# Optimization experiments

Hardware: AMD Instinct MI355X
Metric: run time of the kernel (lower is better)

The kernel has to match this reference:

```python
import jax, jax.numpy as jnp
import numpy as np

EMBED_DIM = 1024
NUM_HEAD = 16
HEAD_DIM = EMBED_DIM // NUM_HEAD
B, T = 4, 2048


def setup_inputs() -> dict:
    key = jax.random.key(0)
    ks = jax.random.split(key, 6)
    s_in = 1.0 / np.sqrt(EMBED_DIM)
    return {
        "hidden_states": jax.random.normal(ks[0], (B, T, EMBED_DIM), dtype=jnp.float32),
        "attn_mask": jnp.ones((B, T), dtype=jnp.int32),
        "W_qkv": jax.random.uniform(ks[1], (3 * EMBED_DIM, EMBED_DIM), jnp.float32, -s_in, s_in),
        "b_qkv": jax.random.uniform(ks[2], (3 * EMBED_DIM,), jnp.float32, -s_in, s_in),
        "W_o": jax.random.uniform(ks[3], (EMBED_DIM, EMBED_DIM), jnp.float32, -s_in, s_in),
        "b_o": jax.random.uniform(ks[4], (EMBED_DIM,), jnp.float32, -s_in, s_in),
    }


def reference(hidden_states, attn_mask, W_qkv, b_qkv, W_o, b_o):
    Bb, Tt, C = hidden_states.shape
    H, D = NUM_HEAD, HEAD_DIM
    scaling = D ** (-0.5)

    qkv = hidden_states @ W_qkv.T + b_qkv  # [B,T,3C]
    q, k, v = jnp.split(qkv, 3, axis=-1)
    # [B,H,T,D]
    q = q.reshape(Bb, Tt, H, D).transpose(0, 2, 1, 3)
    k = k.reshape(Bb, Tt, H, D).transpose(0, 2, 1, 3)
    v = v.reshape(Bb, Tt, H, D).transpose(0, 2, 1, 3)

    scores = jnp.einsum("bhqd,bhkd->bhqk", q, k) * scaling  # [B,H,T,T]

    causal = jnp.tril(jnp.ones((Tt, Tt), dtype=bool))[None, None]  # [1,1,T,T]
    am = attn_mask.astype(bool)
    mask = causal & am[:, None, :, None] & am[:, None, None, :]  # [B,1,T,T]
    scores = jnp.where(mask, scores, -jnp.inf)

    probs = jax.nn.softmax(scores, axis=-1)
    out = jnp.einsum("bhqk,bhkd->bhqd", probs, v)  # [B,H,T,D]
    out = out.transpose(0, 2, 1, 3).reshape(Bb, Tt, C)
    return out @ W_o.T + b_o
```

## Files before the change

kernel.cpp:

```cpp
#include <hip/hip_runtime.h>
#include <cstdint>
#include <cstddef>
#include <math.h>

#define BATCH 4
#define TSEQ  2048
#define CDIM  1024
#define NH    16
#define HDIM  64
#define MTOT  (BATCH * TSEQ)


typedef __attribute__((ext_vector_type(4))) float  floatx4;
typedef __attribute__((ext_vector_type(8))) short  shortx8;
typedef __attribute__((ext_vector_type(4))) short  shortx4;

__device__ __forceinline__ short f2bf(float f) {
    union { float f; unsigned int u; } v; v.f = f;
    unsigned int lsb = (v.u >> 16) & 1u;
    v.u += 0x7fffu + lsb;
    return (short)(v.u >> 16);
}

#if defined(__has_builtin)
#  if __has_builtin(__builtin_amdgcn_exp2f)
#    define EXP2F(x) __builtin_amdgcn_exp2f(x)
#  else
#    define EXP2F(x) exp2f(x)
#  endif
#  if __has_builtin(__builtin_amdgcn_perm)
__device__ __forceinline__ unsigned pack_hi16(unsigned hi, unsigned lo) {
    return __builtin_amdgcn_perm(hi, lo, 0x07060302u);
}
#  else
__device__ __forceinline__ unsigned pack_hi16(unsigned hi, unsigned lo) {
    return (lo >> 16) | (hi & 0xffff0000u);
}
#  endif
#  if __has_builtin(__builtin_amdgcn_mfma_f32_16x16x16bf16_1k)
#    define HAS_MFMA_1K 1
#  else
#    define HAS_MFMA_1K 0
#  endif
#else
#  define EXP2F(x) exp2f(x)
__device__ __forceinline__ unsigned pack_hi16(unsigned hi, unsigned lo) {
    return (lo >> 16) | (hi & 0xffff0000u);
}
#  define HAS_MFMA_1K 0
#endif

#define QSCALE (0.125f * 1.44269504088896f)

__global__ __launch_bounds__(256) void cvt_kernel(const float4* __restrict__ src,
                                                  shortx4* __restrict__ dst, int n4)
{
    int i = blockIdx.x * 256 + threadIdx.x;
    if (i < n4) {
        float4 v = src[i];
        shortx4 s;
        s[0] = f2bf(v.x); s[1] = f2bf(v.y); s[2] = f2bf(v.z); s[3] = f2bf(v.w);
        dst[i] = s;
    }
}

__global__ __launch_bounds__(256) void cvt3_kernel(
    const float4* __restrict__ s1, shortx4* __restrict__ d1,
    const float4* __restrict__ s2, shortx4* __restrict__ d2,
    const float4* __restrict__ s3, shortx4* __restrict__ d3)
{
    int bid = blockIdx.x;
    const float4* s; shortx4* d; int i;
    if (bid < 8192)       { s = s1; d = d1; i = bid * 256 + threadIdx.x; }
    else if (bid < 11264) { s = s2; d = d2; i = (bid - 8192) * 256 + threadIdx.x; }
    else                  { s = s3; d = d3; i = (bid - 11264) * 256 + threadIdx.x; }
    float4 v = s[i];
    shortx4 o;
    o[0] = f2bf(v.x); o[1] = f2bf(v.y); o[2] = f2bf(v.z); o[3] = f2bf(v.w);
    d[i] = o;
}

__device__ __forceinline__ void stageA_bf16(const short* g, short* S, int row0,
                                            int K, int k0, int tid, int wave)
{
#pragma unroll
    for (int i = 0; i < 2; ++i) {
        int c = i * 256 + tid;
        int r = c >> 2, kc = c & 3;
        __builtin_amdgcn_global_load_lds(
            (__attribute__((address_space(1))) void*)(g + (size_t)(row0 + r) * K + k0 + kc * 8),
            (__attribute__((address_space(3))) void*)((char*)S + i * 4096 + wave * 1024),
            16, 0, 0);
    }
}
__device__ __forceinline__ void stageB_f32(const float* g, short* S, int row0,
                                           int K, int k0, int tid)
{
#pragma unroll
    for (int i = 0; i < 4; ++i) {
        int c = i * 256 + tid;
        int r = c >> 3, fc = c & 7;
        const float4 v = *(const float4*)(g + (size_t)(row0 + r) * K + k0 + fc * 4);
        shortx4 s4;
        s4[0] = f2bf(v.x); s4[1] = f2bf(v.y); s4[2] = f2bf(v.z); s4[3] = f2bf(v.w);
        *(shortx4*)(S + r * 32 + fc * 4) = s4;
    }
}

__device__ __forceinline__ void qkv_epilogue(
    floatx4 (&acc)[4][4], const float* bias,
    short* Qo, short* Ko, short* VTo,
    int row0, int col0, int wr, int wc, int quad, int l16)
{
#pragma unroll
    for (int mi = 0; mi < 4; ++mi) {
        int m = row0 + wr * 64 + mi * 16 + quad * 4;
        int b = m >> 11, t0 = m & (TSEQ - 1);
#pragma unroll
        for (int ni = 0; ni < 4; ++ni) {
            int n = col0 + wc * 64 + ni * 16 + l16;
            float bv = bias[n];
            int part = n >> 10, rem = n & 1023;
            int h = rem >> 6, d = rem & 63;
            if (part == 2) {
                shortx4 st;
#pragma unroll
                for (int r = 0; r < 4; ++r) st[r] = f2bf(acc[mi][ni][r] + bv);
                *(shortx4*)(VTo + (((size_t)(b * NH + h)) * HDIM + d) * TSEQ + t0) = st;
            } else {
                short* dst = (part == 0) ? Qo : Ko;
                float scale = (part == 0) ? QSCALE : 1.0f;
#pragma unroll
                for (int r = 0; r < 4; ++r) {
                    size_t idx = (((size_t)(b * NH + h)) * TSEQ + (t0 + r)) * HDIM + d;
                    dst[idx] = f2bf((acc[mi][ni][r] + bv) * scale);
                }
            }
        }
    }
}

__global__ __launch_bounds__(256) void gemm_qkv_fast_kernel(
    const short* __restrict__ A,
    const short* __restrict__ W,
    const float* __restrict__ bias,
    short* __restrict__ Qo, short* __restrict__ Ko, short* __restrict__ VTo)
{
    __shared__ short As[128 * 32];
    __shared__ short Bs[128 * 32];
    const int tid  = threadIdx.x;
    const int lane = tid & 63, wave = tid >> 6;
    const int quad = lane >> 4, l16 = lane & 15;
    const int wr = wave >> 1, wc = wave & 1;
    const int row0 = blockIdx.x * 128;
    const int col0 = blockIdx.y * 128;
    const int K = CDIM;

    floatx4 acc[4][4] = {};

    for (int k0 = 0; k0 < K; k0 += 32) {
        stageA_bf16(A, As, row0, K, k0, tid, wave);
        stageA_bf16(W, Bs, col0, K, k0, tid, wave);
        __syncthreads();

        shortx8 af[4], bfr[4];
#pragma unroll
        for (int mi = 0; mi < 4; ++mi)
            af[mi] = *(const shortx8*)(As + (wr * 64 + mi * 16 + l16) * 32 + quad * 8);
#pragma unroll
        for (int ni = 0; ni < 4; ++ni)
            bfr[ni] = *(const shortx8*)(Bs + (wc * 64 + ni * 16 + l16) * 32 + quad * 8);
#pragma unroll
        for (int mi = 0; mi < 4; ++mi)
#pragma unroll
            for (int ni = 0; ni < 4; ++ni)
                acc[mi][ni] = __builtin_amdgcn_mfma_f32_16x16x32_bf16(
                    af[mi], bfr[ni], acc[mi][ni], 0, 0, 0);
        __syncthreads();
    }
    qkv_epilogue(acc, bias, Qo, Ko, VTo, row0, col0, wr, wc, quad, l16);
}

__global__ __launch_bounds__(256) void gemm_qkv_kernel(
    const short* __restrict__ A,
    const float* __restrict__ W,
    const float* __restrict__ bias,
    short* __restrict__ Qo, short* __restrict__ Ko, short* __restrict__ VTo)
{
    __shared__ short As[128 * 32];
    __shared__ short Bs[128 * 32];
    const int tid  = threadIdx.x;
    const int lane = tid & 63, wave = tid >> 6;
    const int quad = lane >> 4, l16 = lane & 15;
    const int wr = wave >> 1, wc = wave & 1;
    const int row0 = blockIdx.x * 128;
    const int col0 = blockIdx.y * 128;
    const int K = CDIM;

    floatx4 acc[4][4] = {};

    for (int k0 = 0; k0 < K; k0 += 32) {
        stageA_bf16(A, As, row0, K, k0, tid, wave);
        stageB_f32(W, Bs, col0, K, k0, tid);
        __syncthreads();

        shortx8 af[4], bfr[4];
#pragma unroll
        for (int mi = 0; mi < 4; ++mi)
            af[mi] = *(const shortx8*)(As + (wr * 64 + mi * 16 + l16) * 32 + quad * 8);
#pragma unroll
        for (int ni = 0; ni < 4; ++ni)
            bfr[ni] = *(const shortx8*)(Bs + (wc * 64 + ni * 16 + l16) * 32 + quad * 8);
#pragma unroll
        for (int mi = 0; mi < 4; ++mi)
#pragma unroll
            for (int ni = 0; ni < 4; ++ni)
                acc[mi][ni] = __builtin_amdgcn_mfma_f32_16x16x32_bf16(
                    af[mi], bfr[ni], acc[mi][ni], 0, 0, 0);
        __syncthreads();
    }
    qkv_epilogue(acc, bias, Qo, Ko, VTo, row0, col0, wr, wc, quad, l16);
}

__global__ __launch_bounds__(256) void attn_kernel(
    const short* __restrict__ Q,
    const short* __restrict__ Kg,
    const short* __restrict__ VT,
    const int*   __restrict__ am,
    short* __restrict__ O)
{
    __shared__ short Ks[128 * 64];
    __shared__ short Vs[64 * 128];

    const int tid  = threadIdx.x;
    const int lane = tid & 63, wave = tid >> 6;
    const int quad = lane >> 4, l16 = lane & 15;

    const int L = blockIdx.x;
    const int bh = (L & 7) + (((L >> 3) & 7) << 3);
    const int strip = 15 - (L >> 6);
    const int b = bh >> 4, h = bh & 15;

    const short* Qb = Q  + (size_t)bh * TSEQ * HDIM;
    const short* Kb = Kg + (size_t)bh * TSEQ * HDIM;
    const short* Vb = VT + (size_t)bh * HDIM * TSEQ;

    const int q0  = strip * 128;
    const int qb0 = q0 + wave * 32;
    const int qv0 = qb0 + l16;
    const int qv1 = qv0 + 16;

    shortx8 bq[2][2];
#pragma unroll
    for (int nq = 0; nq < 2; ++nq)
#pragma unroll
        for (int kk = 0; kk < 2; ++kk)
            bq[nq][kk] = *(const shortx8*)(
                Qb + (size_t)(qb0 + nq * 16 + l16) * HDIM + kk * 32 + quad * 8);

    floatx4 o[4][2] = {};
    floatx4 lacc[2] = {};

#if HAS_MFMA_1K
    const shortx4 ones4 = { (short)0x3F80, (short)0x3F80, (short)0x3F80, (short)0x3F80 };
#else
    const shortx8 ones8 = { (short)0x3F80, (short)0x3F80, (short)0x3F80, (short)0x3F80,
                            (short)0x3F80, (short)0x3F80, (short)0x3F80, (short)0x3F80 };
#endif

    const int ntiles = (q0 + 128) >> 7;
    for (int kt = 0; kt < ntiles; ++kt) {
        const int kt0 = kt << 7;
#pragma unroll
        for (int i = 0; i < 4; ++i) {
            int idx = i * 256 + tid;
            int rr = idx >> 3, cd = idx & 7;
            int cc = cd ^ (rr & 7);
            __builtin_amdgcn_global_load_lds(
                (__attribute__((address_space(1))) void*)(Kb + (size_t)(kt0 + rr) * HDIM + cc * 8),
                (__attribute__((address_space(3))) void*)((char*)Ks + i * 4096 + wave * 1024),
                16, 0, 0);
            int rrv = idx >> 4, cdv = idx & 15;
            int ccv = cdv ^ (rrv & 7);
            __builtin_amdgcn_global_load_lds(
                (__attribute__((address_space(1))) void*)(Vb + (size_t)rrv * TSEQ + kt0 + ccv * 8),
                (__attribute__((address_space(3))) void*)((char*)Vs + i * 4096 + wave * 1024),
                16, 0, 0);
        }
        int amv0 = am[b * TSEQ + kt0 + lane];
        int amv1 = am[b * TSEQ + kt0 + 64 + lane];
        __syncthreads();

#pragma unroll 1
        for (int p = 0; p < 2; ++p) {
            const int pb0 = kt0 + p * 64;
            int amv = p ? amv1 : amv0;
            bool allones = (__ballot(amv != 0) == 0xFFFFFFFFFFFFFFFFULL);

            floatx4 s[4][2] = {};
#pragma unroll
            for (int kk = 0; kk < 2; ++kk)
#pragma unroll
                for (int t = 0; t < 4; ++t) {
                    int rr = p * 64 + t * 16 + l16;
                    shortx8 kf = *(const shortx8*)(
                        Ks + rr * 64 + (((kk * 4 + quad) ^ (l16 & 7)) << 3));
#pragma unroll
                    for (int nq = 0; nq < 2; ++nq)
                        s[t][nq] = __builtin_amdgcn_mfma_f32_16x16x32_bf16(
                            kf, bq[nq][kk], s[t][nq], 0, 0, 0);
                }

            unsigned pk[4][2][2];
#pragma unroll
            for (int nq = 0; nq < 2; ++nq) {
                const int qv = nq ? qv1 : qv0;
#pragma unroll
                for (int t = 0; t < 4; ++t) {
                    bool diag = (pb0 + t * 16 + 15) > (qb0 + nq * 16);
                    unsigned pu[4];
#pragma unroll
                    for (int r = 0; r < 4; ++r) {
                        float pe = EXP2F(s[t][nq][r]);
                        unsigned u = __float_as_uint(pe) & 0xffff0000u;
                        if (!allones) {
                            int amr = __shfl(amv, t * 16 + quad * 4 + r);
                            u = amr ? u : 0u;
                        }
                        if (diag) {
                            int kv = pb0 + t * 16 + quad * 4 + r;
                            u = (kv <= qv) ? u : 0u;
                        }
                        pu[r] = u;
                    }
                    pk[t][nq][0] = pack_hi16(pu[1], pu[0]);
                    pk[t][nq][1] = pack_hi16(pu[3], pu[2]);
                }
            }

#if HAS_MFMA_1K
#pragma unroll
            for (int t = 0; t < 4; ++t) {
                union { unsigned u[2]; shortx4 s; } pb[2];
                pb[0].u[0] = pk[t][0][0]; pb[0].u[1] = pk[t][0][1];
                pb[1].u[0] = pk[t][1][0]; pb[1].u[1] = pk[t][1][1];
#pragma unroll
                for (int nq = 0; nq < 2; ++nq)
                    lacc[nq] = __builtin_amdgcn_mfma_f32_16x16x16bf16_1k(
                        ones4, pb[nq].s, lacc[nq], 0, 0, 0);
#pragma unroll
                for (int mi = 0; mi < 4; ++mi) {
                    int rr = mi * 16 + l16;
                    int cidx = (p * 8 + 2 * t + (quad >> 1)) ^ (l16 & 7);
                    shortx4 vf = *(const shortx4*)(Vs + rr * 128 + cidx * 8 + (quad & 1) * 4);
#pragma unroll
                    for (int nq = 0; nq < 2; ++nq)
                        o[mi][nq] = __builtin_amdgcn_mfma_f32_16x16x16bf16_1k(
                            vf, pb[nq].s, o[mi][nq], 0, 0, 0);
                }
            }
#else
#pragma unroll
            for (int kk2 = 0; kk2 < 2; ++kk2) {
                unsigned bfr[2][4];
#pragma unroll
                for (int nq = 0; nq < 2; ++nq)
#pragma unroll
                    for (int jj = 0; jj < 4; ++jj) {
                        int srclane = (((quad & 1) * 2 + (jj >> 1)) * 16 + l16) << 2;
                        int lo = __builtin_amdgcn_ds_bpermute(srclane, (int)pk[kk2 * 2][nq][jj & 1]);
                        int hi = __builtin_amdgcn_ds_bpermute(srclane, (int)pk[kk2 * 2 + 1][nq][jj & 1]);
                        bfr[nq][jj] = (quad >> 1) ? (unsigned)hi : (unsigned)lo;
                    }
                union { unsigned u[4]; shortx8 s; } pb[2];
#pragma unroll
                for (int nq = 0; nq < 2; ++nq) {
#pragma unroll
                    for (int jj = 0; jj < 4; ++jj) pb[nq].u[jj] = bfr[nq][jj];
                    lacc[nq] = __builtin_amdgcn_mfma_f32_16x16x32_bf16(
                        ones8, pb[nq].s, lacc[nq], 0, 0, 0);
                }
#pragma unroll
                for (int mi = 0; mi < 4; ++mi) {
                    int rr = mi * 16 + l16;
                    int cidx = (p * 8 + kk2 * 4 + quad) ^ (l16 & 7);
                    shortx8 vf8 = *(const shortx8*)(Vs + rr * 128 + cidx * 8);
#pragma unroll
                    for (int nq = 0; nq < 2; ++nq)
                        o[mi][nq] = __builtin_amdgcn_mfma_f32_16x16x32_bf16(
                            vf8, pb[nq].s, o[mi][nq], 0, 0, 0);
                }
            }
#endif
        }
        __syncthreads();
    }

#pragma unroll
    for (int nq = 0; nq < 2; ++nq) {
        float inv = 1.0f / lacc[nq][0];
        int q = qb0 + nq * 16 + l16;
#pragma unroll
        for (int mi = 0; mi < 4; ++mi) {
            shortx4 st;
#pragma unroll
            for (int r = 0; r < 4; ++r) st[r] = f2bf(o[mi][nq][r] * inv);
            *(shortx4*)(O + ((size_t)(b * TSEQ + q)) * CDIM + h * HDIM + mi * 16 + quad * 4) = st;
        }
    }
}

__global__ __launch_bounds__(256) void gemm_out_kernel(
    const short* __restrict__ A,
    const short* __restrict__ W,
    const float* __restrict__ bias,
    float* __restrict__ Out)
{
    __shared__ short As[128 * 32];
    __shared__ short Bs[128 * 32];
    const int tid  = threadIdx.x;
    const int lane = tid & 63, wave = tid >> 6;
    const int quad = lane >> 4, l16 = lane & 15;
    const int wr = wave >> 1, wc = wave & 1;
    const int row0 = blockIdx.x * 128;
    const int col0 = blockIdx.y * 128;
    const int K = CDIM;

    floatx4 acc[4][4] = {};

    for (int k0 = 0; k0 < K; k0 += 32) {
        stageA_bf16(A, As, row0, K, k0, tid, wave);
        stageA_bf16(W, Bs, col0, K, k0, tid, wave);
        __syncthreads();

        shortx8 af[4], bfr[4];
#pragma unroll
        for (int mi = 0; mi < 4; ++mi)
            af[mi] = *(const shortx8*)(As + (wr * 64 + mi * 16 + l16) * 32 + quad * 8);
#pragma unroll
        for (int ni = 0; ni < 4; ++ni)
            bfr[ni] = *(const shortx8*)(Bs + (wc * 64 + ni * 16 + l16) * 32 + quad * 8);
#pragma unroll
        for (int mi = 0; mi < 4; ++mi)
#pragma unroll
            for (int ni = 0; ni < 4; ++ni)
                acc[mi][ni] = __builtin_amdgcn_mfma_f32_16x16x32_bf16(
                    af[mi], bfr[ni], acc[mi][ni], 0, 0, 0);
        __syncthreads();
    }

#pragma unroll
    for (int mi = 0; mi < 4; ++mi) {
        int m = row0 + wr * 64 + mi * 16 + quad * 4;
#pragma unroll
        for (int ni = 0; ni < 4; ++ni) {
            int n = col0 + wc * 64 + ni * 16 + l16;
            float bv = bias[n];
#pragma unroll
            for (int r = 0; r < 4; ++r)
                Out[(size_t)(m + r) * CDIM + n] = acc[mi][ni][r] + bv;
        }
    }
}

extern "C" void kernel_launch(void* const* d_in, const int* in_sizes, int n_in,
                              void* d_out, int out_size, void* d_ws, size_t ws_size,
                              hipStream_t stream)
{
    const float* hs   = (const float*)d_in[0];
    const int*   am   = (const int*)d_in[1];
    const float* Wqkv = (const float*)d_in[2];
    const float* bqkv = (const float*)d_in[3];
    const float* Wo   = (const float*)d_in[4];
    const float* bo   = (const float*)d_in[5];
    float* out = (float*)d_out;

    char* ws = (char*)d_ws;
    short* slot = (short*)ws;
    short* Qw   = (short*)(ws + ((size_t)16 << 20));
    short* Kw   = (short*)(ws + ((size_t)32 << 20));
    short* VTw  = (short*)(ws + ((size_t)48 << 20));

    if (ws_size >= ((size_t)72 << 20)) {
        short* Wqkvb = (short*)(ws + ((size_t)64 << 20));
        short* Wob   = (short*)(ws + ((size_t)70 << 20));
        cvt3_kernel<<<dim3(12288), 256, 0, stream>>>(
            (const float4*)hs,   (shortx4*)slot,
            (const float4*)Wqkv, (shortx4*)Wqkvb,
            (const float4*)Wo,   (shortx4*)Wob);
        gemm_qkv_fast_kernel<<<dim3(MTOT / 128, (3 * CDIM) / 128), 256, 0, stream>>>(
            slot, Wqkvb, bqkv, Qw, Kw, VTw);
        attn_kernel<<<dim3(1024), 256, 0, stream>>>(
            Qw, Kw, VTw, am, slot);
        gemm_out_kernel<<<dim3(MTOT / 128, CDIM / 128), 256, 0, stream>>>(
            slot, Wob, bo, out);
    } else {
        cvt_kernel<<<dim3((MTOT * CDIM / 4 + 255) / 256), 256, 0, stream>>>(
            (const float4*)hs, (shortx4*)slot, MTOT * CDIM / 4);
        gemm_qkv_kernel<<<dim3(MTOT / 128, (3 * CDIM) / 128), 256, 0, stream>>>(
            slot, Wqkv, bqkv, Qw, Kw, VTw);
        attn_kernel<<<dim3(1024), 256, 0, stream>>>(
            Qw, Kw, VTw, am, slot);
        cvt_kernel<<<dim3((CDIM * CDIM / 4 + 255) / 256), 256, 0, stream>>>(
            (const float4*)Wo, (shortx4*)Kw, CDIM * CDIM / 4);
        gemm_out_kernel<<<dim3(MTOT / 128, CDIM / 128), 256, 0, stream>>>(
            slot, Kw, bo, out);
    }
}
```

Baseline: 275.3 us.

## Rewrite QKV GEMM with 256x256 tiles, double-buffered swizzled LDS and staged prefetch

The fast QKV projection GEMM moves from 128x128 tiles with 4 waves and single-buffered LDS to 256x256 tiles with 8 waves, a K-step of 64 and double-buffered LDS. Direct global-to-LDS loads with an XOR swizzle prefetch the next K tile, interleaved into the four MFMA sub-phases with barriers and setprio. This aims to raise data reuse per loaded byte, hide global load latency, and avoid LDS bank conflicts. It uses 128KB of LDS and many accumulators, so only one block fits per CU, and the grid has just 384 blocks on a large CU count, which risks tail imbalance.

```diff
diff --git a/kernel.cpp b/kernel.cpp
--- a/kernel.cpp
+++ b/kernel.cpp
@@ -107,42 +107,149 @@
     }
 }
 
-__device__ __forceinline__ void qkv_epilogue(
-    floatx4 (&acc)[4][4], const float* bias,
+__device__ __forceinline__ void qkv_scatter(
+    const floatx4& a, const float* bias,
     short* Qo, short* Ko, short* VTo,
-    int row0, int col0, int wr, int wc, int quad, int l16)
-{
-#pragma unroll
-    for (int mi = 0; mi < 4; ++mi) {
-        int m = row0 + wr * 64 + mi * 16 + quad * 4;
-        int b = m >> 11, t0 = m & (TSEQ - 1);
-#pragma unroll
-        for (int ni = 0; ni < 4; ++ni) {
-            int n = col0 + wc * 64 + ni * 16 + l16;
-            float bv = bias[n];
-            int part = n >> 10, rem = n & 1023;
-            int h = rem >> 6, d = rem & 63;
-            if (part == 2) {
-                shortx4 st;
-#pragma unroll
-                for (int r = 0; r < 4; ++r) st[r] = f2bf(acc[mi][ni][r] + bv);
-                *(shortx4*)(VTo + (((size_t)(b * NH + h)) * HDIM + d) * TSEQ + t0) = st;
-            } else {
-                short* dst = (part == 0) ? Qo : Ko;
-                float scale = (part == 0) ? QSCALE : 1.0f;
-#pragma unroll
-                for (int r = 0; r < 4; ++r) {
-                    size_t idx = (((size_t)(b * NH + h)) * TSEQ + (t0 + r)) * HDIM + d;
-                    dst[idx] = f2bf((acc[mi][ni][r] + bv) * scale);
-                }
-            }
-        }
-    }
-}
-
-__global__ __launch_bounds__(256) void gemm_qkv_fast_kernel(
+    int m, int n)
+{
+    float bv = bias[n];
+    int b = m >> 11, t0 = m & (TSEQ - 1);
+    int part = n >> 10, rem = n & 1023;
+    int h = rem >> 6, d = rem & 63;
+    if (part == 2) {
+        shortx4 st;
+#pragma unroll
+        for (int r = 0; r < 4; ++r) st[r] = f2bf(a[r] + bv);
+        *(shortx4*)(VTo + (((size_t)(b * NH + h)) * HDIM + d) * TSEQ + t0) = st;
+    } else {
+        short* dst = (part == 0) ? Qo : Ko;
+        float scale = (part == 0) ? QSCALE : 1.0f;
+#pragma unroll
+        for (int r = 0; r < 4; ++r) {
+            size_t idx = (((size_t)(b * NH + h)) * TSEQ + (t0 + r)) * HDIM + d;
+            dst[idx] = f2bf((a[r] + bv) * scale);
+        }
+    }
+}
+
+__global__ __launch_bounds__(512) void gemm_qkv_fast_kernel(
     const short* __restrict__ A,
     const short* __restrict__ W,
+    const float* __restrict__ bias,
+    short* __restrict__ Qo, short* __restrict__ Ko, short* __restrict__ VTo)
+{
+    __shared__ short lds[2 * 2 * 256 * 64];
+
+    const int tid  = threadIdx.x;
+    const int lane = tid & 63, wid = tid >> 6;
+    const int quad = lane >> 4, l16 = lane & 15;
+    const int wm = wid >> 2, wn = wid & 3;
+    const int row0 = blockIdx.x * 256;
+    const int col0 = blockIdx.y * 256;
+    const int NT = CDIM / 64;
+
+#define GQ_AS1 __attribute__((address_space(1))) void*
+#define GQ_AS3 __attribute__((address_space(3))) void*
+#define STAGE_HALF(gbase, grow0, panel, half, k0)                             \
+    {                                                                         \
+        _Pragma("unroll")                                                     \
+        for (int i = 0; i < 2; ++i) {                                         \
+            int idx = i * 512 + tid;                                          \
+            int rr = idx >> 3, cd = idx & 7;                                  \
+            int cc = cd ^ (rr & 7);                                           \
+            __builtin_amdgcn_global_load_lds(                                 \
+                (GQ_AS1)((gbase) + (size_t)((grow0) + (half) * 128 + rr) * CDIM + (k0) + cc * 8), \
+                (GQ_AS3)((char*)(panel) + (half) * 16384 + i * 8192 + wid * 1024),                \
+                16, 0, 0);                                                    \
+        }                                                                     \
+    }
+
+    floatx4 acc[8][4] = {};
+
+    {
+        short* A0 = lds;
+        short* B0 = lds + 16384;
+        STAGE_HALF(A, row0, A0, 0, 0);
+        STAGE_HALF(A, row0, A0, 1, 0);
+        STAGE_HALF(W, col0, B0, 0, 0);
+        STAGE_HALF(W, col0, B0, 1, 0);
+    }
+    __syncthreads();
+
+    for (int t = 0; t < NT; ++t) {
+        const int bsel = t & 1;
+        const short* Ac = lds + bsel * 32768;
+        const short* Bc = Ac + 16384;
+        short* An = lds + (bsel ^ 1) * 32768;
+        short* Bn = An + 16384;
+        const bool st = (t + 1 < NT);
+        const int k1 = (t + 1) << 6;
+
+        shortx8 bf[4][2];
+#pragma unroll
+        for (int q = 0; q < 4; ++q) {
+            if (q == 0) {
+#pragma unroll
+                for (int ni = 0; ni < 4; ++ni)
+#pragma unroll
+                    for (int ks = 0; ks < 2; ++ks) {
+                        int col = wn * 64 + ni * 16 + l16;
+                        bf[ni][ks] = *(const shortx8*)(
+                            Bc + col * 64 + (((ks * 4 + quad) ^ (l16 & 7)) << 3));
+                    }
+            }
+            shortx8 af[2][2];
+#pragma unroll
+            for (int j = 0; j < 2; ++j)
+#pragma unroll
+                for (int ks = 0; ks < 2; ++ks) {
+                    int row = wm * 128 + (2 * q + j) * 16 + l16;
+                    af[j][ks] = *(const shortx8*)(
+                        Ac + row * 64 + (((ks * 4 + quad) ^ (l16 & 7)) << 3));
+                }
+
+            if (q == 0 && st) {
+                STAGE_HALF(A, row0, An, 0, k1);
+                STAGE_HALF(A, row0, An, 1, k1);
+            }
+            if (q == 1 && st) {
+                STAGE_HALF(W, col0, Bn, 0, k1);
+                STAGE_HALF(W, col0, Bn, 1, k1);
+            }
+
+            __builtin_amdgcn_s_barrier();
+            __builtin_amdgcn_s_setprio(1);
+#pragma unroll
+            for (int j = 0; j < 2; ++j)
+#pragma unroll
+                for (int ni = 0; ni < 4; ++ni)
+#pragma unroll
+                    for (int ks = 0; ks < 2; ++ks)
+                        acc[2 * q + j][ni] = __builtin_amdgcn_mfma_f32_16x16x32_bf16(
+                            af[j][ks], bf[ni][ks], acc[2 * q + j][ni], 0, 0, 0);
+            __builtin_amdgcn_s_setprio(0);
+            if (q < 3) __builtin_amdgcn_s_barrier();
+        }
+        __syncthreads();
+    }
+#undef STAGE_HALF
+#undef GQ_AS1
+#undef GQ_AS3
+
+#pragma unroll
+    for (int mi = 0; mi < 8; ++mi) {
+        int m = row0 + wm * 128 + mi * 16 + quad * 4;
+#pragma unroll
+        for (int ni = 0; ni < 4; ++ni) {
+            int n = col0 + wn * 64 + ni * 16 + l16;
+            qkv_scatter(acc[mi][ni], bias, Qo, Ko, VTo, m, n);
+        }
+    }
+}
+
+__global__ __launch_bounds__(256) void gemm_qkv_kernel(
+    const short* __restrict__ A,
+    const float* __restrict__ W,
     const float* __restrict__ bias,
     short* __restrict__ Qo, short* __restrict__ Ko, short* __restrict__ VTo)
 {
@@ -160,7 +267,7 @@
 
     for (int k0 = 0; k0 < K; k0 += 32) {
         stageA_bf16(A, As, row0, K, k0, tid, wave);
-        stageA_bf16(W, Bs, col0, K, k0, tid, wave);
+        stageB_f32(W, Bs, col0, K, k0, tid);
         __syncthreads();
 
         shortx8 af[4], bfr[4];
@@ -178,48 +285,15 @@
                     af[mi], bfr[ni], acc[mi][ni], 0, 0, 0);
         __syncthreads();
     }
-    qkv_epilogue(acc, bias, Qo, Ko, VTo, row0, col0, wr, wc, quad, l16);
-}
-
-__global__ __launch_bounds__(256) void gemm_qkv_kernel(
-    const short* __restrict__ A,
-    const float* __restrict__ W,
-    const float* __restrict__ bias,
-    short* __restrict__ Qo, short* __restrict__ Ko, short* __restrict__ VTo)
-{
-    __shared__ short As[128 * 32];
-    __shared__ short Bs[128 * 32];
-    const int tid  = threadIdx.x;
-    const int lane = tid & 63, wave = tid >> 6;
-    const int quad = lane >> 4, l16 = lane & 15;
-    const int wr = wave >> 1, wc = wave & 1;
-    const int row0 = blockIdx.x * 128;
-    const int col0 = blockIdx.y * 128;
-    const int K = CDIM;
-
-    floatx4 acc[4][4] = {};
-
-    for (int k0 = 0; k0 < K; k0 += 32) {
-        stageA_bf16(A, As, row0, K, k0, tid, wave);
-        stageB_f32(W, Bs, col0, K, k0, tid);
-        __syncthreads();
-
-        shortx8 af[4], bfr[4];
-#pragma unroll
-        for (int mi = 0; mi < 4; ++mi)
-            af[mi] = *(const shortx8*)(As + (wr * 64 + mi * 16 + l16) * 32 + quad * 8);
-#pragma unroll
-        for (int ni = 0; ni < 4; ++ni)
-            bfr[ni] = *(const shortx8*)(Bs + (wc * 64 + ni * 16 + l16) * 32 + quad * 8);
-#pragma unroll
-        for (int mi = 0; mi < 4; ++mi)
-#pragma unroll
-            for (int ni = 0; ni < 4; ++ni)
-                acc[mi][ni] = __builtin_amdgcn_mfma_f32_16x16x32_bf16(
-                    af[mi], bfr[ni], acc[mi][ni], 0, 0, 0);
-        __syncthreads();
-    }
-    qkv_epilogue(acc, bias, Qo, Ko, VTo, row0, col0, wr, wc, quad, l16);
+#pragma unroll
+    for (int mi = 0; mi < 4; ++mi) {
+        int m = row0 + wr * 64 + mi * 16 + quad * 4;
+#pragma unroll
+        for (int ni = 0; ni < 4; ++ni) {
+            int n = col0 + wc * 64 + ni * 16 + l16;
+            qkv_scatter(acc[mi][ni], bias, Qo, Ko, VTo, m, n);
+        }
+    }
 }
 
 __global__ __launch_bounds__(256) void attn_kernel(
@@ -488,7 +562,7 @@
             (const float4*)hs,   (shortx4*)slot,
             (const float4*)Wqkv, (shortx4*)Wqkvb,
             (const float4*)Wo,   (shortx4*)Wob);
-        gemm_qkv_fast_kernel<<<dim3(MTOT / 128, (3 * CDIM) / 128), 256, 0, stream>>>(
+        gemm_qkv_fast_kernel<<<dim3(MTOT / 256, (3 * CDIM) / 256), 512, 0, stream>>>(
             slot, Wqkvb, bqkv, Qw, Kw, VTw);
         attn_kernel<<<dim3(1024), 256, 0, stream>>>(
             Qw, Kw, VTw, am, slot);
```

New measurement: 267.4 us. 2.9% less time.
